# Kernel tuning notes

Measured on AMD Instinct MI355X. Metric: run time of the kernel, lower is better.

Reference implementation:

```python
import jax, jax.numpy as jnp
import numpy as np

N_QUBITS = 6
N_LAYERS = 6
DIM = 2 ** N_QUBITS  # 64


def _qft_matrix():
    # PennyLane qml.QFT matrix: F[j,k] = exp(2*pi*i*j*k/N) / sqrt(N)
    j = np.arange(DIM)
    F = np.exp(2j * np.pi * np.outer(j, j) / DIM) / np.sqrt(DIM)
    return jnp.asarray(F, dtype=jnp.complex64)


def _cnot_ring_perm():
    # Composite permutation of basis states for CNOT(q, (q+1)%n) applied q=0..n-1.
    # Wire 0 is the most significant bit (PennyLane convention).
    m = np.arange(DIM)
    for q in range(N_QUBITS):
        c_bit = N_QUBITS - 1 - q
        t_bit = N_QUBITS - 1 - ((q + 1) % N_QUBITS)
        ctrl = (m >> c_bit) & 1
        m = np.where(ctrl == 1, m ^ (1 << t_bit), m)
    # state_out[m_final] = state_in[m_init]  ->  gather index = argsort(m)
    return jnp.asarray(np.argsort(m), dtype=jnp.int32)


_QFT = _qft_matrix()
_CNOT_PERM = _cnot_ring_perm()


def _layer_unitary(thetas):
    # kron of per-qubit RY(theta) gates (they act on distinct wires -> single 64x64 matrix)
    c = jnp.cos(thetas / 2.0)
    s = jnp.sin(thetas / 2.0)
    U = jnp.array(1.0, dtype=thetas.dtype).reshape(1, 1)
    for q in range(N_QUBITS):
        g = jnp.stack([jnp.stack([c[q], -s[q]]), jnp.stack([s[q], c[q]])])  # [2,2]
        U = jnp.kron(U, g)
    return U.astype(jnp.complex64)  # [64,64]


def setup_inputs() -> dict:
    key = jax.random.key(0)
    k1, k2 = jax.random.split(key)
    x = jax.random.normal(k1, (65536, DIM), dtype=jnp.float32)
    weights_rot = jax.random.normal(k2, (N_LAYERS, N_QUBITS), dtype=jnp.float32) * 0.01
    return {"x": x, "weights_rot": weights_rot}


def reference(x, weights_rot):
    # AmplitudeEmbedding with normalize=True
    norm = jnp.sqrt(jnp.sum(x * x, axis=-1, keepdims=True))
    psi = (x / norm).astype(jnp.complex64)  # [B, 64]
    # QFT on all wires
    psi = jnp.einsum('jk,bk->bj', _QFT, psi)
    # layers: fused RY-on-all-wires unitary, then CNOT ring permutation
    for l in range(N_LAYERS):
        U = _layer_unitary(weights_rot[l])
        psi = jnp.einsum('ij,bj->bi', U, psi)
        psi = jnp.take(psi, _CNOT_PERM, axis=1)
    # probs over all wires
    return psi.real ** 2 + psi.imag ** 2  # [B, 64] float32
```

## Files before the change

### kernel.cpp

```cpp
#include <hip/hip_runtime.h>
#include <hip/hip_bf16.h>

#define NQ 6
#define DIM 64
#define NLAYERS 6

typedef __attribute__((ext_vector_type(8))) short bf16x8;
typedef __attribute__((ext_vector_type(4))) float f32x4;

__global__ __launch_bounds__(64) void build_M(const float* __restrict__ w,
                                              unsigned short* __restrict__ Bf) {
    const int k = blockIdx.x;
    const int j = threadIdx.x;

    int t = (j * k) & 63;
    float sv, cv;
    sincospif((float)t / 32.0f, &sv, &cv);
    float vr = cv * 0.125f;
    float vi = sv * 0.125f;

    int m = j;
#pragma unroll
    for (int q = 0; q < NQ; ++q) {
        int cb = 5 - q;
        int tb = 5 - ((q + 1) % NQ);
        if ((m >> cb) & 1) m ^= (1 << tb);
    }
    const int dst4 = m << 2;

    for (int l = 0; l < NLAYERS; ++l) {
#pragma unroll
        for (int q = 0; q < NQ; ++q) {
            float th = w[l * NQ + q] * 0.5f;
            float c = cosf(th), s = sinf(th);
            int b = 5 - q;
            float pr = __shfl_xor(vr, 1 << b);
            float pi = __shfl_xor(vi, 1 << b);
            float sgn = ((j >> b) & 1) ? s : -s;
            vr = c * vr + sgn * pr;
            vi = c * vi + sgn * pi;
        }
        vr = __int_as_float(__builtin_amdgcn_ds_permute(dst4, __float_as_int(vr)));
        vi = __int_as_float(__builtin_amdgcn_ds_permute(dst4, __float_as_int(vi)));
    }

    const int jt = j >> 4;
    const int lane16 = (j & 15) + 16 * ((k >> 3) & 3);
    const int chunk = k >> 5;
    const int e = k & 7;
    const int base = ((jt * 2 + chunk) * 4) * 512 + lane16 * 8 + e;

    __hip_bfloat16 rh = __float2bfloat16(vr);
    __hip_bfloat16 rl = __float2bfloat16(vr - __bfloat162float(rh));
    __hip_bfloat16 ih = __float2bfloat16(vi);
    __hip_bfloat16 il = __float2bfloat16(vi - __bfloat162float(ih));
    Bf[base]        = *(unsigned short*)&rh;
    Bf[base + 512]  = *(unsigned short*)&rl;
    Bf[base + 1024] = *(unsigned short*)&ih;
    Bf[base + 1536] = *(unsigned short*)&il;
}

__global__ __launch_bounds__(256) void qenc_main(const float* __restrict__ x,
                                                 const unsigned short* __restrict__ Bf,
                                                 float* __restrict__ out) {
    __shared__ __align__(16) unsigned short sB[16384];
    const int tid = threadIdx.x;

    {
        const float4* src = (const float4*)Bf;
        float4* dst = (float4*)sB;
#pragma unroll
        for (int i = 0; i < 8; ++i) dst[tid + 256 * i] = src[tid + 256 * i];
    }

    const int lane = tid & 63;
    const int wid = tid >> 6;
    const int row0 = blockIdx.x * 64 + wid * 16;
    const int r = lane & 15;
    const int g = lane >> 4;

    const float* xp = x + (size_t)(row0 + r) * DIM + 8 * g;
    float xf[16];
    *(float4*)(xf)      = *(const float4*)(xp);
    *(float4*)(xf + 4)  = *(const float4*)(xp + 4);
    *(float4*)(xf + 8)  = *(const float4*)(xp + 32);
    *(float4*)(xf + 12) = *(const float4*)(xp + 36);

    float p2 = 0.f;
#pragma unroll
    for (int i = 0; i < 16; ++i) p2 = fmaf(xf[i], xf[i], p2);
    p2 += __shfl_xor(p2, 16);
    p2 += __shfl_xor(p2, 32);
    const float inv = 1.0f / p2;

    bf16x8 ah[2], al[2];
#pragma unroll
    for (int c = 0; c < 2; ++c)
#pragma unroll
        for (int i = 0; i < 8; ++i) {
            float f = xf[c * 8 + i];
            __hip_bfloat16 h = __float2bfloat16(f);
            __hip_bfloat16 lo = __float2bfloat16(f - __bfloat162float(h));
            ah[c][i] = *(short*)&h;
            al[c][i] = *(short*)&lo;
        }

    __syncthreads();

    const f32x4 z = {0.f, 0.f, 0.f, 0.f};
    f32x4 acr[4] = {z, z, z, z};
    f32x4 aci[4] = {z, z, z, z};
    const unsigned short* bp = sB + lane * 8;

#pragma unroll
    for (int jt = 0; jt < 4; ++jt) {
#pragma unroll
        for (int c = 0; c < 2; ++c) {
            const unsigned short* fb = bp + ((jt * 2 + c) * 4) * 512;
            bf16x8 brh = *(const bf16x8*)(fb);
            bf16x8 brl = *(const bf16x8*)(fb + 512);
            bf16x8 bih = *(const bf16x8*)(fb + 1024);
            bf16x8 bil = *(const bf16x8*)(fb + 1536);
            acr[jt] = __builtin_amdgcn_mfma_f32_16x16x32_bf16(ah[c], brh, acr[jt], 0, 0, 0);
            acr[jt] = __builtin_amdgcn_mfma_f32_16x16x32_bf16(ah[c], brl, acr[jt], 0, 0, 0);
            acr[jt] = __builtin_amdgcn_mfma_f32_16x16x32_bf16(al[c], brh, acr[jt], 0, 0, 0);
            aci[jt] = __builtin_amdgcn_mfma_f32_16x16x32_bf16(ah[c], bih, aci[jt], 0, 0, 0);
            aci[jt] = __builtin_amdgcn_mfma_f32_16x16x32_bf16(ah[c], bil, aci[jt], 0, 0, 0);
            aci[jt] = __builtin_amdgcn_mfma_f32_16x16x32_bf16(al[c], bih, aci[jt], 0, 0, 0);
        }
    }

    float invv[4];
#pragma unroll
    for (int v = 0; v < 4; ++v) invv[v] = __shfl(inv, 4 * g + v);

    float* op = out + (size_t)(row0 + 4 * g) * DIM + r;
#pragma unroll
    for (int v = 0; v < 4; ++v)
#pragma unroll
        for (int jt = 0; jt < 4; ++jt) {
            float yr = acr[jt][v];
            float yi = aci[jt][v];
            op[(size_t)v * DIM + jt * 16] = (yr * yr + yi * yi) * invv[v];
        }
}

extern "C" void kernel_launch(void* const* d_in, const int* in_sizes, int n_in,
                              void* d_out, int out_size, void* d_ws, size_t ws_size,
                              hipStream_t stream) {
    const float* x = (const float*)d_in[0];
    const float* w = (const float*)d_in[1];
    float* out = (float*)d_out;
    unsigned short* Bf = (unsigned short*)d_ws;
    int B = in_sizes[0] / DIM;

    hipLaunchKernelGGL(build_M, dim3(DIM), dim3(64), 0, stream, w, Bf);
    hipLaunchKernelGGL(qenc_main, dim3(B / 64), dim3(256), 0, stream, x, Bf, out);
}
```

Before: 20.94 us.

## Drop LDS staging of B and process two row tiles per wave

The main kernel no longer copies the 32 KB B matrix into shared memory and syncs. Each wave now reads B fragments straight from global memory, relying on L2/L1 caching. Each wave handles 32 rows instead of 16, so every B fragment load feeds twice as many MFMAs and the grid is halved. The cost is more registers per thread (doubled accumulators and A fragments) and dependence on cache hits for the repeated B reads.

```diff
diff --git a/kernel.cpp b/kernel.cpp
--- a/kernel.cpp
+++ b/kernel.cpp
@@ -60,88 +60,101 @@
     Bf[base + 1536] = *(unsigned short*)&il;
 }
 
+__device__ __forceinline__ void split8(const float* f, bf16x8& h, bf16x8& l) {
+#pragma unroll
+    for (int i = 0; i < 8; ++i) {
+        __hip_bfloat16 hh = __float2bfloat16(f[i]);
+        __hip_bfloat16 ll = __float2bfloat16(f[i] - __bfloat162float(hh));
+        h[i] = *(short*)&hh;
+        l[i] = *(short*)&ll;
+    }
+}
+
 __global__ __launch_bounds__(256) void qenc_main(const float* __restrict__ x,
                                                  const unsigned short* __restrict__ Bf,
                                                  float* __restrict__ out) {
-    __shared__ __align__(16) unsigned short sB[16384];
     const int tid = threadIdx.x;
-
-    {
-        const float4* src = (const float4*)Bf;
-        float4* dst = (float4*)sB;
-#pragma unroll
-        for (int i = 0; i < 8; ++i) dst[tid + 256 * i] = src[tid + 256 * i];
-    }
-
     const int lane = tid & 63;
     const int wid = tid >> 6;
-    const int row0 = blockIdx.x * 64 + wid * 16;
+    const int row0 = blockIdx.x * 128 + wid * 32;
     const int r = lane & 15;
     const int g = lane >> 4;
 
-    const float* xp = x + (size_t)(row0 + r) * DIM + 8 * g;
-    float xf[16];
-    *(float4*)(xf)      = *(const float4*)(xp);
-    *(float4*)(xf + 4)  = *(const float4*)(xp + 4);
-    *(float4*)(xf + 8)  = *(const float4*)(xp + 32);
-    *(float4*)(xf + 12) = *(const float4*)(xp + 36);
+    const float* xp0 = x + (size_t)(row0 + r) * DIM + 8 * g;
+    const float* xp1 = xp0 + (size_t)16 * DIM;
+    float xf0[16], xf1[16];
+    *(float4*)(xf0)      = *(const float4*)(xp0);
+    *(float4*)(xf0 + 4)  = *(const float4*)(xp0 + 4);
+    *(float4*)(xf0 + 8)  = *(const float4*)(xp0 + 32);
+    *(float4*)(xf0 + 12) = *(const float4*)(xp0 + 36);
+    *(float4*)(xf1)      = *(const float4*)(xp1);
+    *(float4*)(xf1 + 4)  = *(const float4*)(xp1 + 4);
+    *(float4*)(xf1 + 8)  = *(const float4*)(xp1 + 32);
+    *(float4*)(xf1 + 12) = *(const float4*)(xp1 + 36);
 
-    float p2 = 0.f;
+    float n0 = 0.f, n1 = 0.f;
 #pragma unroll
-    for (int i = 0; i < 16; ++i) p2 = fmaf(xf[i], xf[i], p2);
-    p2 += __shfl_xor(p2, 16);
-    p2 += __shfl_xor(p2, 32);
-    const float inv = 1.0f / p2;
+    for (int i = 0; i < 16; ++i) {
+        n0 = fmaf(xf0[i], xf0[i], n0);
+        n1 = fmaf(xf1[i], xf1[i], n1);
+    }
+    n0 += __shfl_xor(n0, 16);  n0 += __shfl_xor(n0, 32);
+    n1 += __shfl_xor(n1, 16);  n1 += __shfl_xor(n1, 32);
+    const float inv0 = 1.0f / n0;
+    const float inv1 = 1.0f / n1;
 
-    bf16x8 ah[2], al[2];
-#pragma unroll
-    for (int c = 0; c < 2; ++c)
-#pragma unroll
-        for (int i = 0; i < 8; ++i) {
-            float f = xf[c * 8 + i];
-            __hip_bfloat16 h = __float2bfloat16(f);
-            __hip_bfloat16 lo = __float2bfloat16(f - __bfloat162float(h));
-            ah[c][i] = *(short*)&h;
-            al[c][i] = *(short*)&lo;
-        }
-
-    __syncthreads();
+    bf16x8 a0h[2], a0l[2], a1h[2], a1l[2];
+    split8(xf0,     a0h[0], a0l[0]);
+    split8(xf0 + 8, a0h[1], a0l[1]);
+    split8(xf1,     a1h[0], a1l[0]);
+    split8(xf1 + 8, a1h[1], a1l[1]);
 
     const f32x4 z = {0.f, 0.f, 0.f, 0.f};
-    f32x4 acr[4] = {z, z, z, z};
-    f32x4 aci[4] = {z, z, z, z};
-    const unsigned short* bp = sB + lane * 8;
+    f32x4 acr0[4] = {z, z, z, z}, aci0[4] = {z, z, z, z};
+    f32x4 acr1[4] = {z, z, z, z}, aci1[4] = {z, z, z, z};
+    const bf16x8* bb = (const bf16x8*)Bf + lane;
 
 #pragma unroll
     for (int jt = 0; jt < 4; ++jt) {
 #pragma unroll
         for (int c = 0; c < 2; ++c) {
-            const unsigned short* fb = bp + ((jt * 2 + c) * 4) * 512;
-            bf16x8 brh = *(const bf16x8*)(fb);
-            bf16x8 brl = *(const bf16x8*)(fb + 512);
-            bf16x8 bih = *(const bf16x8*)(fb + 1024);
-            bf16x8 bil = *(const bf16x8*)(fb + 1536);
-            acr[jt] = __builtin_amdgcn_mfma_f32_16x16x32_bf16(ah[c], brh, acr[jt], 0, 0, 0);
-            acr[jt] = __builtin_amdgcn_mfma_f32_16x16x32_bf16(ah[c], brl, acr[jt], 0, 0, 0);
-            acr[jt] = __builtin_amdgcn_mfma_f32_16x16x32_bf16(al[c], brh, acr[jt], 0, 0, 0);
-            aci[jt] = __builtin_amdgcn_mfma_f32_16x16x32_bf16(ah[c], bih, aci[jt], 0, 0, 0);
-            aci[jt] = __builtin_amdgcn_mfma_f32_16x16x32_bf16(ah[c], bil, aci[jt], 0, 0, 0);
-            aci[jt] = __builtin_amdgcn_mfma_f32_16x16x32_bf16(al[c], bih, aci[jt], 0, 0, 0);
+            const int f0 = (jt * 2 + c) * 4;
+            bf16x8 brh = bb[(f0 + 0) * 64];
+            bf16x8 brl = bb[(f0 + 1) * 64];
+            bf16x8 bih = bb[(f0 + 2) * 64];
+            bf16x8 bil = bb[(f0 + 3) * 64];
+            acr0[jt] = __builtin_amdgcn_mfma_f32_16x16x32_bf16(a0h[c], brh, acr0[jt], 0, 0, 0);
+            acr0[jt] = __builtin_amdgcn_mfma_f32_16x16x32_bf16(a0h[c], brl, acr0[jt], 0, 0, 0);
+            acr0[jt] = __builtin_amdgcn_mfma_f32_16x16x32_bf16(a0l[c], brh, acr0[jt], 0, 0, 0);
+            aci0[jt] = __builtin_amdgcn_mfma_f32_16x16x32_bf16(a0h[c], bih, aci0[jt], 0, 0, 0);
+            aci0[jt] = __builtin_amdgcn_mfma_f32_16x16x32_bf16(a0h[c], bil, aci0[jt], 0, 0, 0);
+            aci0[jt] = __builtin_amdgcn_mfma_f32_16x16x32_bf16(a0l[c], bih, aci0[jt], 0, 0, 0);
+            acr1[jt] = __builtin_amdgcn_mfma_f32_16x16x32_bf16(a1h[c], brh, acr1[jt], 0, 0, 0);
+            acr1[jt] = __builtin_amdgcn_mfma_f32_16x16x32_bf16(a1h[c], brl, acr1[jt], 0, 0, 0);
+            acr1[jt] = __builtin_amdgcn_mfma_f32_16x16x32_bf16(a1l[c], brh, acr1[jt], 0, 0, 0);
+            aci1[jt] = __builtin_amdgcn_mfma_f32_16x16x32_bf16(a1h[c], bih, aci1[jt], 0, 0, 0);
+            aci1[jt] = __builtin_amdgcn_mfma_f32_16x16x32_bf16(a1h[c], bil, aci1[jt], 0, 0, 0);
+            aci1[jt] = __builtin_amdgcn_mfma_f32_16x16x32_bf16(a1l[c], bih, aci1[jt], 0, 0, 0);
         }
     }
 
-    float invv[4];
+    float iv0[4], iv1[4];
 #pragma unroll
-    for (int v = 0; v < 4; ++v) invv[v] = __shfl(inv, 4 * g + v);
+    for (int v = 0; v < 4; ++v) {
+        iv0[v] = __shfl(inv0, 4 * g + v);
+        iv1[v] = __shfl(inv1, 4 * g + v);
+    }
 
-    float* op = out + (size_t)(row0 + 4 * g) * DIM + r;
+    float* op0 = out + (size_t)(row0 + 4 * g) * DIM + r;
+    float* op1 = op0 + (size_t)16 * DIM;
 #pragma unroll
     for (int v = 0; v < 4; ++v)
 #pragma unroll
         for (int jt = 0; jt < 4; ++jt) {
-            float yr = acr[jt][v];
-            float yi = aci[jt][v];
-            op[(size_t)v * DIM + jt * 16] = (yr * yr + yi * yi) * invv[v];
+            float yr0 = acr0[jt][v], yi0 = aci0[jt][v];
+            float yr1 = acr1[jt][v], yi1 = aci1[jt][v];
+            op0[(size_t)v * DIM + jt * 16] = (yr0 * yr0 + yi0 * yi0) * iv0[v];
+            op1[(size_t)v * DIM + jt * 16] = (yr1 * yr1 + yi1 * yi1) * iv1[v];
         }
 }
 
@@ -155,5 +168,5 @@
     int B = in_sizes[0] / DIM;
 
     hipLaunchKernelGGL(build_M, dim3(DIM), dim3(64), 0, stream, w, Bf);
-    hipLaunchKernelGGL(qenc_main, dim3(B / 64), dim3(256), 0, stream, x, Bf, out);
+    hipLaunchKernelGGL(qenc_main, dim3(B / 128), dim3(256), 0, stream, x, Bf, out);
 }
```

New measurement: 22.72 us. 1.08x slower.

## Swap MFMA operand roles, read matrix from global, vectorize output stores

Applied to the files above, without the earlier changes.

Removes the shared-memory staging of the 32KB transform matrix and the block barrier, and loads matrix fragments straight from global memory, relying on cache since every block reads the same data. The MFMA operands are swapped so the matrix is the A operand and x is the B operand, which transposes the accumulator layout. Each lane now holds four consecutive output columns for its own row, so it writes float4 stores and no longer needs the shuffle of the inverse norm. The trade-off is repeated global/L2 loads of the matrix per wave in place of a single LDS fill per block.

```diff
diff --git a/kernel.cpp b/kernel.cpp
--- a/kernel.cpp
+++ b/kernel.cpp
@@ -60,19 +60,20 @@
     Bf[base + 1536] = *(unsigned short*)&il;
 }
 
+__device__ __forceinline__ void split8(const float* f, bf16x8& h, bf16x8& l) {
+#pragma unroll
+    for (int i = 0; i < 8; ++i) {
+        __hip_bfloat16 hh = __float2bfloat16(f[i]);
+        __hip_bfloat16 ll = __float2bfloat16(f[i] - __bfloat162float(hh));
+        h[i] = *(short*)&hh;
+        l[i] = *(short*)&ll;
+    }
+}
+
 __global__ __launch_bounds__(256) void qenc_main(const float* __restrict__ x,
                                                  const unsigned short* __restrict__ Bf,
                                                  float* __restrict__ out) {
-    __shared__ __align__(16) unsigned short sB[16384];
     const int tid = threadIdx.x;
-
-    {
-        const float4* src = (const float4*)Bf;
-        float4* dst = (float4*)sB;
-#pragma unroll
-        for (int i = 0; i < 8; ++i) dst[tid + 256 * i] = src[tid + 256 * i];
-    }
-
     const int lane = tid & 63;
     const int wid = tid >> 6;
     const int row0 = blockIdx.x * 64 + wid * 16;
@@ -86,63 +87,50 @@
     *(float4*)(xf + 8)  = *(const float4*)(xp + 32);
     *(float4*)(xf + 12) = *(const float4*)(xp + 36);
 
-    float p2 = 0.f;
+    float n0 = 0.f;
 #pragma unroll
-    for (int i = 0; i < 16; ++i) p2 = fmaf(xf[i], xf[i], p2);
-    p2 += __shfl_xor(p2, 16);
-    p2 += __shfl_xor(p2, 32);
-    const float inv = 1.0f / p2;
+    for (int i = 0; i < 16; ++i) n0 = fmaf(xf[i], xf[i], n0);
+    n0 += __shfl_xor(n0, 16);
+    n0 += __shfl_xor(n0, 32);
+    const float inv = 1.0f / n0;
 
-    bf16x8 ah[2], al[2];
-#pragma unroll
-    for (int c = 0; c < 2; ++c)
-#pragma unroll
-        for (int i = 0; i < 8; ++i) {
-            float f = xf[c * 8 + i];
-            __hip_bfloat16 h = __float2bfloat16(f);
-            __hip_bfloat16 lo = __float2bfloat16(f - __bfloat162float(h));
-            ah[c][i] = *(short*)&h;
-            al[c][i] = *(short*)&lo;
-        }
-
-    __syncthreads();
+    bf16x8 xh[2], xl[2];
+    split8(xf,     xh[0], xl[0]);
+    split8(xf + 8, xh[1], xl[1]);
 
     const f32x4 z = {0.f, 0.f, 0.f, 0.f};
     f32x4 acr[4] = {z, z, z, z};
     f32x4 aci[4] = {z, z, z, z};
-    const unsigned short* bp = sB + lane * 8;
+    const bf16x8* bb = (const bf16x8*)Bf + lane;
 
 #pragma unroll
     for (int jt = 0; jt < 4; ++jt) {
 #pragma unroll
         for (int c = 0; c < 2; ++c) {
-            const unsigned short* fb = bp + ((jt * 2 + c) * 4) * 512;
-            bf16x8 brh = *(const bf16x8*)(fb);
-            bf16x8 brl = *(const bf16x8*)(fb + 512);
-            bf16x8 bih = *(const bf16x8*)(fb + 1024);
-            bf16x8 bil = *(const bf16x8*)(fb + 1536);
-            acr[jt] = __builtin_amdgcn_mfma_f32_16x16x32_bf16(ah[c], brh, acr[jt], 0, 0, 0);
-            acr[jt] = __builtin_amdgcn_mfma_f32_16x16x32_bf16(ah[c], brl, acr[jt], 0, 0, 0);
-            acr[jt] = __builtin_amdgcn_mfma_f32_16x16x32_bf16(al[c], brh, acr[jt], 0, 0, 0);
-            aci[jt] = __builtin_amdgcn_mfma_f32_16x16x32_bf16(ah[c], bih, aci[jt], 0, 0, 0);
-            aci[jt] = __builtin_amdgcn_mfma_f32_16x16x32_bf16(ah[c], bil, aci[jt], 0, 0, 0);
-            aci[jt] = __builtin_amdgcn_mfma_f32_16x16x32_bf16(al[c], bih, aci[jt], 0, 0, 0);
+            const int f0 = (jt * 2 + c) * 4;
+            bf16x8 mrh = bb[(f0 + 0) * 64];
+            bf16x8 mrl = bb[(f0 + 1) * 64];
+            bf16x8 mih = bb[(f0 + 2) * 64];
+            bf16x8 mil = bb[(f0 + 3) * 64];
+            acr[jt] = __builtin_amdgcn_mfma_f32_16x16x32_bf16(mrh, xh[c], acr[jt], 0, 0, 0);
+            acr[jt] = __builtin_amdgcn_mfma_f32_16x16x32_bf16(mrh, xl[c], acr[jt], 0, 0, 0);
+            acr[jt] = __builtin_amdgcn_mfma_f32_16x16x32_bf16(mrl, xh[c], acr[jt], 0, 0, 0);
+            aci[jt] = __builtin_amdgcn_mfma_f32_16x16x32_bf16(mih, xh[c], aci[jt], 0, 0, 0);
+            aci[jt] = __builtin_amdgcn_mfma_f32_16x16x32_bf16(mih, xl[c], aci[jt], 0, 0, 0);
+            aci[jt] = __builtin_amdgcn_mfma_f32_16x16x32_bf16(mil, xh[c], aci[jt], 0, 0, 0);
         }
     }
 
-    float invv[4];
+    float* op = out + (size_t)(row0 + r) * DIM + 4 * g;
 #pragma unroll
-    for (int v = 0; v < 4; ++v) invv[v] = __shfl(inv, 4 * g + v);
-
-    float* op = out + (size_t)(row0 + 4 * g) * DIM + r;
-#pragma unroll
-    for (int v = 0; v < 4; ++v)
-#pragma unroll
-        for (int jt = 0; jt < 4; ++jt) {
-            float yr = acr[jt][v];
-            float yi = aci[jt][v];
-            op[(size_t)v * DIM + jt * 16] = (yr * yr + yi * yi) * invv[v];
-        }
+    for (int jt = 0; jt < 4; ++jt) {
+        float4 o;
+        o.x = (acr[jt][0] * acr[jt][0] + aci[jt][0] * aci[jt][0]) * inv;
+        o.y = (acr[jt][1] * acr[jt][1] + aci[jt][1] * aci[jt][1]) * inv;
+        o.z = (acr[jt][2] * acr[jt][2] + aci[jt][2] * aci[jt][2]) * inv;
+        o.w = (acr[jt][3] * acr[jt][3] + aci[jt][3] * aci[jt][3]) * inv;
+        *(float4*)(op + jt * 16) = o;
+    }
 }
 
 extern "C" void kernel_launch(void* const* d_in, const int* in_sizes, int n_in,
```

After: 24.52 us. +17.1%, slower.
